# Optimization experiments

Hardware: AMD Instinct MI355X
Metric: run time of the kernel (lower is better)

## Reference

```python
import jax, jax.numpy as jnp
import numpy as np

B, S, D = 4, 2048, 1024
E, ES, K = 16, 256, 4  # n_experts, expert_size, top-k (= n_heads)
STD_GATE = 0.02


def setup_inputs() -> dict:
    key = jax.random.key(0)
    k1, k2, k3, k4 = jax.random.split(key, 4)
    x = jax.random.normal(k1, (B, S, D), dtype=jnp.float32)
    # init per module: gate ~ N(0, d^-0.5), keys ~ N(0, d^-0.5), values ~ N(0, size^-0.5)
    w_gate = jax.random.normal(k2, (E, D), dtype=jnp.float32) * (D ** -0.5)
    keys = jax.random.normal(k3, (E, D, ES), dtype=jnp.float32) * (D ** -0.5)
    values = jax.random.normal(k4, (E, ES, D), dtype=jnp.float32) * ((E * ES) ** -0.5)
    return {"x": x, "w_gate": w_gate, "keys": keys, "values": values}


def reference(x, w_gate, keys, values):
    # sigma-MoE forward (selection_mode='sigmoid', activation=relu,
    # num_selected = n_heads = K, no bias, no dropout, eval mode)
    xt = x.reshape(-1, D)                         # [T, D]
    T = xt.shape[0]
    logits = xt @ w_gate.T                        # [T, E]
    sel = jax.nn.sigmoid(logits)                  # sigmoid gating
    sel_val, sel_idx = jax.lax.top_k(sel, K)      # [T, K]
    # sparse gate weights as dense [T, E] mask (zeros for unselected experts)
    gate_w = jnp.zeros((T, E), dtype=x.dtype).at[
        jnp.arange(T)[:, None], sel_idx
    ].set(sel_val)
    # per-expert hidden: h[t,e,s] = relu(sum_d x[t,d] keys[e,d,s])
    h = jax.nn.relu(jnp.einsum('td,eds->tes', xt, keys))  # [T, E, ES]
    # weighted scatter back through values: out = sum_e gate * h_e @ values_e
    out = jnp.einsum('tes,te,esv->tv', h, gate_w, values)  # [T, D]
    return out.reshape(B, S, D)
```

## Files before the change

### kernel.cpp

```cpp
#include <hip/hip_runtime.h>
#include <hip/hip_bf16.h>
#include <stdint.h>

#define T_TOK 8192
#define DIM   1024
#define NEXP  16
#define ESZ   256
#define TOPK  4
#define BM    128
#define BK    64
#define NPAIR (T_TOK*TOPK)
#define NBLK  128
#define MAXROWS (T_TOK*TOPK + NEXP*BM)
#define MAXTILES (T_TOK*TOPK/BM + NEXP)

typedef __hip_bfloat16 bf16;
typedef short bf16x8 __attribute__((ext_vector_type(8)));
typedef float f32x4 __attribute__((ext_vector_type(4)));

__device__ __forceinline__ unsigned short f2bu(float f){
  __hip_bfloat16 b = __float2bfloat16(f);
  return *reinterpret_cast<unsigned short*>(&b);
}
__device__ __forceinline__ float bu2f(unsigned short u){
  __hip_bfloat16 b = *reinterpret_cast<__hip_bfloat16*>(&u);
  return __bfloat162float(b);
}

__device__ __forceinline__ void gload16(const void* g, void* l){
  __builtin_amdgcn_global_load_lds((const __attribute__((address_space(1))) void*)g,
                                   (__attribute__((address_space(3))) void*)l, 16, 0, 0);
}

__global__ __launch_bounds__(256) void k_gate(const float* __restrict__ x,
    const float* __restrict__ wg, bf16* __restrict__ xb,
    int* __restrict__ sel_idx, float* __restrict__ sel_gate)
{
  const int wave = threadIdx.x >> 6, lane = threadIdx.x & 63;
  const int t = blockIdx.x*4 + wave;
  const float* xr = x + (size_t)t*DIM;
  float4 xv[4];
#pragma unroll
  for (int c=0;c<4;c++) xv[c] = *(const float4*)(xr + c*256 + lane*4);
#pragma unroll
  for (int c=0;c<4;c++){
    ushort4 o; o.x=f2bu(xv[c].x); o.y=f2bu(xv[c].y); o.z=f2bu(xv[c].z); o.w=f2bu(xv[c].w);
    *(ushort4*)((unsigned short*)xb + (size_t)t*DIM + c*256 + lane*4) = o;
  }
  float sg[NEXP];
#pragma unroll
  for (int e=0;e<NEXP;e++){
    const float* wr = wg + e*DIM;
    float p = 0.f;
#pragma unroll
    for (int c=0;c<4;c++){
      float4 w = *(const float4*)(wr + c*256 + lane*4);
      p += xv[c].x*w.x + xv[c].y*w.y + xv[c].z*w.z + xv[c].w*w.w;
    }
#pragma unroll
    for (int s=1;s<64;s<<=1) p += __shfl_xor(p, s);
    sg[e] = 1.f/(1.f + expf(-p));
  }
  if (lane==0){
    unsigned chosen = 0;
#pragma unroll
    for (int k=0;k<TOPK;k++){
      float best=-1.f; int bi=0;
#pragma unroll
      for (int e=0;e<NEXP;e++){
        float v = ((chosen>>e)&1u) ? -2.f : sg[e];
        if (v>best){best=v;bi=e;}
      }
      chosen |= 1u<<bi;
      sel_idx[t*TOPK+k]=bi; sel_gate[t*TOPK+k]=best;
    }
  }
}

__global__ __launch_bounds__(256) void k_transpose2(const float* __restrict__ keys,
    const float* __restrict__ values, bf16* __restrict__ kT, bf16* __restrict__ vT)
{
  __shared__ float tile[32][33];
  const int which = blockIdx.y >> 4, e = blockIdx.y & 15;
  const int R = which ? ESZ : DIM, C = which ? DIM : ESZ;
  const float* src = (which ? values : keys) + (size_t)e*DIM*ESZ;
  bf16* dst = (which ? vT : kT) + (size_t)e*DIM*ESZ;
  const int ctiles = C/32;
  const int r0 = (blockIdx.x / ctiles)*32, c0 = (blockIdx.x % ctiles)*32;
  const int tx = threadIdx.x & 31, ty = threadIdx.x >> 5;
#pragma unroll
  for (int i=0;i<4;i++){ int r = ty + i*8; tile[r][tx] = src[(size_t)(r0+r)*C + c0 + tx]; }
  __syncthreads();
#pragma unroll
  for (int i=0;i<4;i++){ int r = ty + i*8; dst[(size_t)(c0+r)*R + r0 + tx] = __float2bfloat16(tile[tx][r]); }
}

__global__ __launch_bounds__(256) void k_hist(const int* __restrict__ sel_idx,
    int* __restrict__ block_hist)
{
  __shared__ int h[NEXP];
  if (threadIdx.x < NEXP) h[threadIdx.x]=0;
  __syncthreads();
  atomicAdd(&h[sel_idx[blockIdx.x*256 + threadIdx.x]], 1);
  __syncthreads();
  if (threadIdx.x < NEXP) block_hist[blockIdx.x*NEXP + threadIdx.x] = h[threadIdx.x];
}

__global__ void k_meta(const int* __restrict__ block_hist,
    int* __restrict__ tile_expert, int* __restrict__ tile_rowstart,
    int* __restrict__ tile_segend, int* __restrict__ block_base)
{
  __shared__ int cnt[NEXP], seg[NEXP];
  const int tid = threadIdx.x;
  if (tid < NEXP){
    int s=0;
    for (int b=0;b<NBLK;b++) s += block_hist[b*NEXP + tid];
    cnt[tid]=s;
  }
  __syncthreads();
  if (tid==0){
    int off=0, tc=0;
    for (int e=0;e<NEXP;e++){
      seg[e]=off;
      int c = cnt[e];
      int nt = (c + BM - 1)/BM;
      for (int i=0;i<nt;i++){
        tile_expert[tc]=e; tile_rowstart[tc]=off+i*BM; tile_segend[tc]=off+c; tc++;
      }
      off += nt*BM;
    }
    for (; tc<MAXTILES; tc++) tile_expert[tc]=-1;
  }
  __syncthreads();
  if (tid < NEXP){
    int s = seg[tid];
    for (int b=0;b<NBLK;b++){ block_base[b*NEXP + tid] = s; s += block_hist[b*NEXP + tid]; }
  }
}

__global__ __launch_bounds__(256) void k_scatter(const int* __restrict__ sel_idx,
    const float* __restrict__ sel_gate, const int* __restrict__ block_base,
    int* __restrict__ assign_token, float* __restrict__ assign_gate,
    int* __restrict__ inv_rows)
{
  __shared__ int wcnt[4][NEXP];
  const int p = blockIdx.x*256 + threadIdx.x;
  const int wave = threadIdx.x >> 6, lane = threadIdx.x & 63;
  const int e = sel_idx[p];
  const float g = sel_gate[p];
  int rank = 0;
#pragma unroll
  for (int ee=0; ee<NEXP; ee++){
    unsigned long long m = __ballot(e==ee);
    if (lane==0) wcnt[wave][ee] = (int)__popcll(m);
    if (e==ee) rank = (int)__popcll(m & ((1ull<<lane)-1ull));
  }
  __syncthreads();
  int pre = 0;
  for (int w=0; w<wave; w++) pre += wcnt[w][e];
  const int row = block_base[blockIdx.x*NEXP + e] + pre + rank;
  assign_token[row] = p >> 2;
  assign_gate[row]  = g;
  inv_rows[p] = row;
}

__global__ __launch_bounds__(256) void k_gemm1(
    const bf16* __restrict__ xb, const bf16* __restrict__ kT,
    const int* __restrict__ assign_token, const float* __restrict__ assign_gate,
    const int* __restrict__ tile_expert, const int* __restrict__ tile_rowstart,
    const int* __restrict__ tile_segend, bf16* __restrict__ h)
{
  __shared__ char smem[65536];
  __shared__ int   tokens_s[BM];
  __shared__ float gates_s[BM];

  const int nb = blockIdx.x, tile = blockIdx.y;
  const int e = tile_expert[tile];
  if (e < 0) return;
  const int row0 = tile_rowstart[tile];
  const int segend = tile_segend[tile];
  const int tid = threadIdx.x, wave = tid>>6, lane = tid&63;

  if (tid < BM){
    int rg = row0 + tid;
    bool vld = rg < segend;
    tokens_s[tid] = vld ? assign_token[rg] : 0;
    gates_s[tid]  = vld ? assign_gate[rg] : 0.f;
  }
  __syncthreads();

  char* As = smem;
  char* Bs = smem + 32768;
  const bf16* gA[4]; const bf16* gB[4]; int lo[4];
#pragma unroll
  for (int i=0;i<4;i++){
    int rl = (wave*4+i)*8 + (lane>>3);
    int c  = (lane&7) ^ (rl&7);
    gA[i] = xb + (size_t)tokens_s[rl]*DIM + c*8;
    gB[i] = kT + ((size_t)e*ESZ + nb*BM + rl)*DIM + c*8;
    lo[i] = (wave*4+i)*1024;
  }

  f32x4 acc[4][4];
#pragma unroll
  for (int m=0;m<4;m++)
#pragma unroll
    for (int n=0;n<4;n++) acc[m][n] = {0.f,0.f,0.f,0.f};

  const int wr0 = (wave>>1)*64, wc0 = (wave&1)*64;
  const int NT = DIM/BK;

#pragma unroll
  for (int i=0;i<4;i++){ gload16(gA[i], As + lo[i]); gload16(gB[i], Bs + lo[i]); }
  asm volatile("s_waitcnt vmcnt(0)" ::: "memory");
  __builtin_amdgcn_s_barrier();

  for (int kt=0; kt<NT; ++kt){
    const int cur = kt & 1;
    if (kt+1 < NT){
      const int nxt = cur^1;
#pragma unroll
      for (int i=0;i<4;i++){
        gload16(gA[i] + (kt+1)*BK, As + nxt*16384 + lo[i]);
        gload16(gB[i] + (kt+1)*BK, Bs + nxt*16384 + lo[i]);
      }
    }
    const char* Ab = As + cur*16384; const char* Bb = Bs + cur*16384;
#pragma unroll
    for (int kk=0;kk<2;kk++){
      bf16x8 af[4], bfr[4];
#pragma unroll
      for (int m=0;m<4;m++){
        int row = wr0 + m*16 + (lane&15);
        int kb  = kk*64 + (lane>>4)*16;
        af[m] = *(const bf16x8*)(Ab + row*128 + (kb ^ ((row&7)<<4)));
      }
#pragma unroll
      for (int n=0;n<4;n++){
        int col = wc0 + n*16 + (lane&15);
        int kb  = kk*64 + (lane>>4)*16;
        bfr[n] = *(const bf16x8*)(Bb + col*128 + (kb ^ ((col&7)<<4)));
      }
#pragma unroll
      for (int m=0;m<4;m++)
#pragma unroll
        for (int n=0;n<4;n++)
          acc[m][n] = __builtin_amdgcn_mfma_f32_16x16x32_bf16(af[m], bfr[n], acc[m][n], 0,0,0);
    }
    asm volatile("s_waitcnt vmcnt(0)" ::: "memory");
    __builtin_amdgcn_s_barrier();
  }

#pragma unroll
  for (int m=0;m<4;m++)
#pragma unroll
    for (int n=0;n<4;n++){
      int col = wc0 + n*16 + (lane&15);
#pragma unroll
      for (int j=0;j<4;j++){
        int rloc = wr0 + m*16 + ((lane>>4)<<2) + j;
        float v = fmaxf(acc[m][n][j], 0.f) * gates_s[rloc];
        h[(size_t)(row0 + rloc)*ESZ + nb*BM + col] = __float2bfloat16(v);
      }
    }
}

__global__ __launch_bounds__(256) void k_gemm2(
    const bf16* __restrict__ h, const bf16* __restrict__ vT,
    const int* __restrict__ tile_expert, const int* __restrict__ tile_rowstart,
    bf16* __restrict__ partial)
{
  __shared__ char smem[65536];

  const int nb = blockIdx.x, tile = blockIdx.y;
  const int e = tile_expert[tile];
  if (e < 0) return;
  const int row0 = tile_rowstart[tile];
  const int tid = threadIdx.x, wave = tid>>6, lane = tid&63;

  char* As = smem;
  char* Bs = smem + 32768;
  const bf16* gA[4]; const bf16* gB[4]; int lo[4];
#pragma unroll
  for (int i=0;i<4;i++){
    int rl = (wave*4+i)*8 + (lane>>3);
    int c  = (lane&7) ^ (rl&7);
    gA[i] = h + (size_t)(row0 + rl)*ESZ + c*8;
    gB[i] = vT + ((size_t)e*DIM + nb*BM + rl)*ESZ + c*8;
    lo[i] = (wave*4+i)*1024;
  }

  f32x4 acc[4][4];
#pragma unroll
  for (int m=0;m<4;m++)
#pragma unroll
    for (int n=0;n<4;n++) acc[m][n] = {0.f,0.f,0.f,0.f};

  const int wr0 = (wave>>1)*64, wc0 = (wave&1)*64;
  const int NT = ESZ/BK;

#pragma unroll
  for (int i=0;i<4;i++){ gload16(gA[i], As + lo[i]); gload16(gB[i], Bs + lo[i]); }
  asm volatile("s_waitcnt vmcnt(0)" ::: "memory");
  __builtin_amdgcn_s_barrier();

  for (int kt=0; kt<NT; ++kt){
    const int cur = kt & 1;
    if (kt+1 < NT){
      const int nxt = cur^1;
#pragma unroll
      for (int i=0;i<4;i++){
        gload16(gA[i] + (kt+1)*BK, As + nxt*16384 + lo[i]);
        gload16(gB[i] + (kt+1)*BK, Bs + nxt*16384 + lo[i]);
      }
    }
    const char* Ab = As + cur*16384; const char* Bb = Bs + cur*16384;
#pragma unroll
    for (int kk=0;kk<2;kk++){
      bf16x8 af[4], bfr[4];
#pragma unroll
      for (int m=0;m<4;m++){
        int row = wr0 + m*16 + (lane&15);
        int kb  = kk*64 + (lane>>4)*16;
        af[m] = *(const bf16x8*)(Ab + row*128 + (kb ^ ((row&7)<<4)));
      }
#pragma unroll
      for (int n=0;n<4;n++){
        int col = wc0 + n*16 + (lane&15);
        int kb  = kk*64 + (lane>>4)*16;
        bfr[n] = *(const bf16x8*)(Bb + col*128 + (kb ^ ((col&7)<<4)));
      }
#pragma unroll
      for (int m=0;m<4;m++)
#pragma unroll
        for (int n=0;n<4;n++)
          acc[m][n] = __builtin_amdgcn_mfma_f32_16x16x32_bf16(af[m], bfr[n], acc[m][n], 0,0,0);
    }
    asm volatile("s_waitcnt vmcnt(0)" ::: "memory");
    __builtin_amdgcn_s_barrier();
  }

#pragma unroll
  for (int m=0;m<4;m++)
#pragma unroll
    for (int n=0;n<4;n++){
      int col = wc0 + n*16 + (lane&15);
#pragma unroll
      for (int j=0;j<4;j++){
        int rloc = wr0 + m*16 + ((lane>>4)<<2) + j;
        partial[(size_t)(row0 + rloc)*DIM + nb*BM + col] = __float2bfloat16(acc[m][n][j]);
      }
    }
}

__global__ __launch_bounds__(256) void k_reduce(const bf16* __restrict__ partial,
    const int* __restrict__ inv_rows, float* __restrict__ out)
{
  const int t = blockIdx.x;
  const int c0 = threadIdx.x * 4;
  int rows[TOPK];
#pragma unroll
  for (int k=0;k<TOPK;k++) rows[k] = inv_rows[t*TOPK+k];
  float a0=0.f,a1=0.f,a2=0.f,a3=0.f;
#pragma unroll
  for (int k=0;k<TOPK;k++){
    ushort4 v = *(const ushort4*)((const unsigned short*)partial + (size_t)rows[k]*DIM + c0);
    a0 += bu2f(v.x); a1 += bu2f(v.y); a2 += bu2f(v.z); a3 += bu2f(v.w);
  }
  float4 o = {a0,a1,a2,a3};
  *(float4*)(out + (size_t)t*DIM + c0) = o;
}

extern "C" void kernel_launch(void* const* d_in, const int* in_sizes, int n_in,
                              void* d_out, int out_size, void* d_ws, size_t ws_size,
                              hipStream_t stream)
{
  const float* x      = (const float*)d_in[0];
  const float* wg     = (const float*)d_in[1];
  const float* keys   = (const float*)d_in[2];
  const float* values = (const float*)d_in[3];
  float* out = (float*)d_out;

  char* ws = (char*)d_ws;
  size_t off = 0;
  bf16* vT   = (bf16*)(ws+off); off += (size_t)NEXP*DIM*ESZ*2;
  bf16* hbuf = (bf16*)(ws+off); off += (size_t)MAXROWS*ESZ*2;
  int*   sel_idx      = (int*)  (ws+off); off += (size_t)NPAIR*4;
  float* sel_gate     = (float*)(ws+off); off += (size_t)NPAIR*4;
  int*   assign_token = (int*)  (ws+off); off += (size_t)MAXROWS*4;
  float* assign_gate  = (float*)(ws+off); off += (size_t)MAXROWS*4;
  int*   inv_rows     = (int*)  (ws+off); off += (size_t)NPAIR*4;
  int*   block_hist   = (int*)  (ws+off); off += (size_t)NBLK*NEXP*4;
  int*   block_base   = (int*)  (ws+off); off += (size_t)NBLK*NEXP*4;
  int*   tile_expert  = (int*)  (ws+off); off += 4096;
  int*   tile_rowstart= (int*)  (ws+off); off += 4096;
  int*   tile_segend  = (int*)  (ws+off); off += 4096;
  const size_t PARTIAL_BYTES = (size_t)MAXROWS*DIM*2;
  const size_t XB_BYTES = (size_t)T_TOK*DIM*2;
  const size_t KT_BYTES = (size_t)NEXP*ESZ*DIM*2;
  bf16* partial = (bf16*)(ws+off); off += PARTIAL_BYTES;
  bf16* xb = (bf16*)((char*)partial + PARTIAL_BYTES - XB_BYTES - KT_BYTES);
  bf16* kT = (bf16*)((char*)partial + PARTIAL_BYTES - KT_BYTES);

  k_gate<<<T_TOK/4, 256, 0, stream>>>(x, wg, xb, sel_idx, sel_gate);
  k_transpose2<<<dim3(256, NEXP*2), 256, 0, stream>>>(keys, values, kT, vT);
  k_hist<<<NBLK, 256, 0, stream>>>(sel_idx, block_hist);
  k_meta<<<1, 256, 0, stream>>>(block_hist, tile_expert, tile_rowstart, tile_segend, block_base);
  k_scatter<<<NBLK, 256, 0, stream>>>(sel_idx, sel_gate, block_base, assign_token,
      assign_gate, inv_rows);
  k_gemm1<<<dim3(ESZ/BM, MAXTILES), 256, 0, stream>>>(xb, kT, assign_token, assign_gate,
      tile_expert, tile_rowstart, tile_segend, hbuf);
  k_gemm2<<<dim3(DIM/BM, MAXTILES), 256, 0, stream>>>(hbuf, vT,
      tile_expert, tile_rowstart, partial);
  k_reduce<<<T_TOK, 256, 0, stream>>>(partial, inv_rows, out);
}
```

Before: 164.6 us.

## Fuse expert up and down GEMMs into one kernel keeping hidden tile in LDS

Merges the two grouped GEMM kernels into a single 512-thread kernel. Each block computes the full 128x256 hidden tile for its expert, applies relu and the gate, stores it swizzled in shared memory, then streams the value weights to produce all 1024 output columns. This removes the global round trip of the hidden buffer and the recomputation of token gathers across column blocks. In exchange each block needs 96KB of LDS, so fewer blocks fit per CU and there is less parallelism per tile. It also remaps tile indices for scheduling.

```diff
diff --git a/kernel.cpp b/kernel.cpp
--- a/kernel.cpp
+++ b/kernel.cpp
@@ -164,17 +164,19 @@
   inv_rows[p] = row;
 }
 
-__global__ __launch_bounds__(256) void k_gemm1(
+__global__ __launch_bounds__(512) void k_expert(
     const bf16* __restrict__ xb, const bf16* __restrict__ kT,
+    const bf16* __restrict__ vT,
     const int* __restrict__ assign_token, const float* __restrict__ assign_gate,
     const int* __restrict__ tile_expert, const int* __restrict__ tile_rowstart,
-    const int* __restrict__ tile_segend, bf16* __restrict__ h)
-{
-  __shared__ char smem[65536];
+    const int* __restrict__ tile_segend, bf16* __restrict__ partial)
+{
+  __shared__ char smem[98304];
   __shared__ int   tokens_s[BM];
   __shared__ float gates_s[BM];
 
-  const int nb = blockIdx.x, tile = blockIdx.y;
+  const int bid = blockIdx.x;
+  const int tile = (bid & 7)*34 + (bid >> 3);
   const int e = tile_expert[tile];
   if (e < 0) return;
   const int row0 = tile_rowstart[tile];
@@ -185,20 +187,28 @@
     int rg = row0 + tid;
     bool vld = rg < segend;
     tokens_s[tid] = vld ? assign_token[rg] : 0;
-    gates_s[tid]  = vld ? assign_gate[rg] : 0.f;
+    gates_s[tid]  = vld ? assign_gate[rg]  : 0.f;
   }
   __syncthreads();
 
   char* As = smem;
   char* Bs = smem + 32768;
-  const bf16* gA[4]; const bf16* gB[4]; int lo[4];
+
+  const bf16* gA[2]; int loA[2];
+#pragma unroll
+  for (int i=0;i<2;i++){
+    int r = wave*16 + i*8 + (lane>>3);
+    int c = (lane&7) ^ (r&7);
+    gA[i] = xb + (size_t)tokens_s[r]*DIM + c*8;
+    loA[i] = (wave*2+i)*1024;
+  }
+  const bf16* gB[4]; int loB[4];
 #pragma unroll
   for (int i=0;i<4;i++){
-    int rl = (wave*4+i)*8 + (lane>>3);
-    int c  = (lane&7) ^ (rl&7);
-    gA[i] = xb + (size_t)tokens_s[rl]*DIM + c*8;
-    gB[i] = kT + ((size_t)e*ESZ + nb*BM + rl)*DIM + c*8;
-    lo[i] = (wave*4+i)*1024;
+    int col = wave*32 + i*8 + (lane>>3);
+    int c = (lane&7) ^ (col&7);
+    gB[i] = kT + ((size_t)e*ESZ + col)*DIM + c*8;
+    loB[i] = (wave*4+i)*1024;
   }
 
   f32x4 acc[4][4];
@@ -207,25 +217,26 @@
 #pragma unroll
     for (int n=0;n<4;n++) acc[m][n] = {0.f,0.f,0.f,0.f};
 
-  const int wr0 = (wave>>1)*64, wc0 = (wave&1)*64;
-  const int NT = DIM/BK;
-
-#pragma unroll
-  for (int i=0;i<4;i++){ gload16(gA[i], As + lo[i]); gload16(gB[i], Bs + lo[i]); }
+  const int wr0 = (wave>>2)*64, wc0 = (wave&3)*64;
+
+#pragma unroll
+  for (int i=0;i<2;i++) gload16(gA[i], As + loA[i]);
+#pragma unroll
+  for (int i=0;i<4;i++) gload16(gB[i], Bs + loB[i]);
   asm volatile("s_waitcnt vmcnt(0)" ::: "memory");
   __builtin_amdgcn_s_barrier();
 
-  for (int kt=0; kt<NT; ++kt){
+  for (int kt=0; kt<16; ++kt){
     const int cur = kt & 1;
-    if (kt+1 < NT){
+    if (kt < 15){
       const int nxt = cur^1;
 #pragma unroll
-      for (int i=0;i<4;i++){
-        gload16(gA[i] + (kt+1)*BK, As + nxt*16384 + lo[i]);
-        gload16(gB[i] + (kt+1)*BK, Bs + nxt*16384 + lo[i]);
-      }
-    }
-    const char* Ab = As + cur*16384; const char* Bb = Bs + cur*16384;
+      for (int i=0;i<2;i++) gload16(gA[i] + (kt+1)*BK, As + nxt*16384 + loA[i]);
+#pragma unroll
+      for (int i=0;i<4;i++) gload16(gB[i] + (kt+1)*BK, Bs + nxt*32768 + loB[i]);
+    }
+    const char* Ab = As + cur*16384;
+    const char* Bb = Bs + cur*32768;
 #pragma unroll
     for (int kk=0;kk<2;kk++){
       bf16x8 af[4], bfr[4];
@@ -251,6 +262,19 @@
     __builtin_amdgcn_s_barrier();
   }
 
+  char* h_s = smem;
+  char* Vs  = smem + 65536;
+  const bf16* gV[2]; int loV[2];
+#pragma unroll
+  for (int i=0;i<2;i++){
+    int vr = wave*16 + i*8 + (lane>>3);
+    int c  = (lane&7) ^ (vr&7);
+    gV[i] = vT + ((size_t)e*DIM + vr)*ESZ + c*8;
+    loV[i] = (wave*2+i)*1024;
+  }
+#pragma unroll
+  for (int i=0;i<2;i++) gload16(gV[i], Vs + loV[i]);
+
 #pragma unroll
   for (int m=0;m<4;m++)
 #pragma unroll
@@ -258,99 +282,71 @@
       int col = wc0 + n*16 + (lane&15);
 #pragma unroll
       for (int j=0;j<4;j++){
-        int rloc = wr0 + m*16 + ((lane>>4)<<2) + j;
-        float v = fmaxf(acc[m][n][j], 0.f) * gates_s[rloc];
-        h[(size_t)(row0 + rloc)*ESZ + nb*BM + col] = __float2bfloat16(v);
-      }
-    }
-}
-
-__global__ __launch_bounds__(256) void k_gemm2(
-    const bf16* __restrict__ h, const bf16* __restrict__ vT,
-    const int* __restrict__ tile_expert, const int* __restrict__ tile_rowstart,
-    bf16* __restrict__ partial)
-{
-  __shared__ char smem[65536];
-
-  const int nb = blockIdx.x, tile = blockIdx.y;
-  const int e = tile_expert[tile];
-  if (e < 0) return;
-  const int row0 = tile_rowstart[tile];
-  const int tid = threadIdx.x, wave = tid>>6, lane = tid&63;
-
-  char* As = smem;
-  char* Bs = smem + 32768;
-  const bf16* gA[4]; const bf16* gB[4]; int lo[4];
-#pragma unroll
-  for (int i=0;i<4;i++){
-    int rl = (wave*4+i)*8 + (lane>>3);
-    int c  = (lane&7) ^ (rl&7);
-    gA[i] = h + (size_t)(row0 + rl)*ESZ + c*8;
-    gB[i] = vT + ((size_t)e*DIM + nb*BM + rl)*ESZ + c*8;
-    lo[i] = (wave*4+i)*1024;
-  }
-
-  f32x4 acc[4][4];
+        int row = wr0 + m*16 + ((lane>>4)<<2) + j;
+        float v = fmaxf(acc[m][n][j], 0.f) * gates_s[row];
+        *(unsigned short*)(h_s + row*512 + ((col*2) ^ ((row&7)<<4))) = f2bu(v);
+      }
+    }
+  asm volatile("s_waitcnt vmcnt(0) lgkmcnt(0)" ::: "memory");
+  __builtin_amdgcn_s_barrier();
+
+  f32x4 acc2[4][2];
 #pragma unroll
   for (int m=0;m<4;m++)
 #pragma unroll
-    for (int n=0;n<4;n++) acc[m][n] = {0.f,0.f,0.f,0.f};
-
-  const int wr0 = (wave>>1)*64, wc0 = (wave&1)*64;
-  const int NT = ESZ/BK;
-
-#pragma unroll
-  for (int i=0;i<4;i++){ gload16(gA[i], As + lo[i]); gload16(gB[i], Bs + lo[i]); }
-  asm volatile("s_waitcnt vmcnt(0)" ::: "memory");
-  __builtin_amdgcn_s_barrier();
-
-  for (int kt=0; kt<NT; ++kt){
-    const int cur = kt & 1;
-    if (kt+1 < NT){
+    for (int n=0;n<2;n++) acc2[m][n] = {0.f,0.f,0.f,0.f};
+  const int qr0 = (wave>>2)*64;
+  const int qc0 = (wave&3)*32;
+
+  for (int s=0; s<32; ++s){
+    const int cur = s & 1;
+    if (s+1 < 32){
       const int nxt = cur^1;
-#pragma unroll
-      for (int i=0;i<4;i++){
-        gload16(gA[i] + (kt+1)*BK, As + nxt*16384 + lo[i]);
-        gload16(gB[i] + (kt+1)*BK, Bs + nxt*16384 + lo[i]);
-      }
-    }
-    const char* Ab = As + cur*16384; const char* Bb = Bs + cur*16384;
+      const int off = ((s+1)>>2)*32768 + ((s+1)&3)*64;
+#pragma unroll
+      for (int i=0;i<2;i++) gload16(gV[i] + off, Vs + nxt*16384 + loV[i]);
+    }
+    const char* Vb = Vs + cur*16384;
+    const int kt = s & 3;
 #pragma unroll
     for (int kk=0;kk<2;kk++){
-      bf16x8 af[4], bfr[4];
+      bf16x8 af[4], bfr[2];
 #pragma unroll
       for (int m=0;m<4;m++){
-        int row = wr0 + m*16 + (lane&15);
-        int kb  = kk*64 + (lane>>4)*16;
-        af[m] = *(const bf16x8*)(Ab + row*128 + (kb ^ ((row&7)<<4)));
-      }
-#pragma unroll
-      for (int n=0;n<4;n++){
-        int col = wc0 + n*16 + (lane&15);
-        int kb  = kk*64 + (lane>>4)*16;
-        bfr[n] = *(const bf16x8*)(Bb + col*128 + (kb ^ ((col&7)<<4)));
+        int vr = qr0 + m*16 + (lane&15);
+        int kb = kk*64 + (lane>>4)*16;
+        af[m] = *(const bf16x8*)(Vb + vr*128 + (kb ^ ((vr&7)<<4)));
+      }
+#pragma unroll
+      for (int n=0;n<2;n++){
+        int tok = qc0 + n*16 + (lane&15);
+        int hb  = kt*128 + kk*64 + (lane>>4)*16;
+        bfr[n] = *(const bf16x8*)(h_s + tok*512 + (hb ^ ((tok&7)<<4)));
       }
 #pragma unroll
       for (int m=0;m<4;m++)
 #pragma unroll
-        for (int n=0;n<4;n++)
-          acc[m][n] = __builtin_amdgcn_mfma_f32_16x16x32_bf16(af[m], bfr[n], acc[m][n], 0,0,0);
+        for (int n=0;n<2;n++)
+          acc2[m][n] = __builtin_amdgcn_mfma_f32_16x16x32_bf16(af[m], bfr[n], acc2[m][n], 0,0,0);
+    }
+    if (kt == 3){
+      const int chunk = s >> 2;
+#pragma unroll
+      for (int m=0;m<4;m++)
+#pragma unroll
+        for (int n=0;n<2;n++){
+          int tok = qc0 + n*16 + (lane&15);
+          int od  = chunk*128 + qr0 + m*16 + ((lane>>4)<<2);
+          ushort4 o;
+          o.x = f2bu(acc2[m][n][0]); o.y = f2bu(acc2[m][n][1]);
+          o.z = f2bu(acc2[m][n][2]); o.w = f2bu(acc2[m][n][3]);
+          *(ushort4*)((unsigned short*)partial + (size_t)(row0+tok)*DIM + od) = o;
+          acc2[m][n] = {0.f,0.f,0.f,0.f};
+        }
     }
     asm volatile("s_waitcnt vmcnt(0)" ::: "memory");
     __builtin_amdgcn_s_barrier();
   }
-
-#pragma unroll
-  for (int m=0;m<4;m++)
-#pragma unroll
-    for (int n=0;n<4;n++){
-      int col = wc0 + n*16 + (lane&15);
-#pragma unroll
-      for (int j=0;j<4;j++){
-        int rloc = wr0 + m*16 + ((lane>>4)<<2) + j;
-        partial[(size_t)(row0 + rloc)*DIM + nb*BM + col] = __float2bfloat16(acc[m][n][j]);
-      }
-    }
 }
 
 __global__ __launch_bounds__(256) void k_reduce(const bf16* __restrict__ partial,
@@ -384,7 +380,8 @@
   char* ws = (char*)d_ws;
   size_t off = 0;
   bf16* vT   = (bf16*)(ws+off); off += (size_t)NEXP*DIM*ESZ*2;
-  bf16* hbuf = (bf16*)(ws+off); off += (size_t)MAXROWS*ESZ*2;
+  bf16* kT   = (bf16*)(ws+off); off += (size_t)NEXP*ESZ*DIM*2;
+  bf16* xb   = (bf16*)(ws+off); off += (size_t)T_TOK*DIM*2;
   int*   sel_idx      = (int*)  (ws+off); off += (size_t)NPAIR*4;
   float* sel_gate     = (float*)(ws+off); off += (size_t)NPAIR*4;
   int*   assign_token = (int*)  (ws+off); off += (size_t)MAXROWS*4;
@@ -395,12 +392,7 @@
   int*   tile_expert  = (int*)  (ws+off); off += 4096;
   int*   tile_rowstart= (int*)  (ws+off); off += 4096;
   int*   tile_segend  = (int*)  (ws+off); off += 4096;
-  const size_t PARTIAL_BYTES = (size_t)MAXROWS*DIM*2;
-  const size_t XB_BYTES = (size_t)T_TOK*DIM*2;
-  const size_t KT_BYTES = (size_t)NEXP*ESZ*DIM*2;
-  bf16* partial = (bf16*)(ws+off); off += PARTIAL_BYTES;
-  bf16* xb = (bf16*)((char*)partial + PARTIAL_BYTES - XB_BYTES - KT_BYTES);
-  bf16* kT = (bf16*)((char*)partial + PARTIAL_BYTES - KT_BYTES);
+  bf16* partial = (bf16*)(ws+off); off += (size_t)MAXROWS*DIM*2;
 
   k_gate<<<T_TOK/4, 256, 0, stream>>>(x, wg, xb, sel_idx, sel_gate);
   k_transpose2<<<dim3(256, NEXP*2), 256, 0, stream>>>(keys, values, kT, vT);
@@ -408,9 +400,7 @@
   k_meta<<<1, 256, 0, stream>>>(block_hist, tile_expert, tile_rowstart, tile_segend, block_base);
   k_scatter<<<NBLK, 256, 0, stream>>>(sel_idx, sel_gate, block_base, assign_token,
       assign_gate, inv_rows);
-  k_gemm1<<<dim3(ESZ/BM, MAXTILES), 256, 0, stream>>>(xb, kT, assign_token, assign_gate,
-      tile_expert, tile_rowstart, tile_segend, hbuf);
-  k_gemm2<<<dim3(DIM/BM, MAXTILES), 256, 0, stream>>>(hbuf, vT,
-      tile_expert, tile_rowstart, partial);
+  k_expert<<<MAXTILES, 512, 0, stream>>>(xb, kT, vT, assign_token, assign_gate,
+      tile_expert, tile_rowstart, tile_segend, partial);
   k_reduce<<<T_TOK, 256, 0, stream>>>(partial, inv_rows, out);
 }
```

Measured after the change: 202.3 us. 1.23x slower.

## Fuse expert histogram into gate kernel and restructure GEMM double-buffer loops

Applied to the files above, without the earlier changes.

The per-block expert histogram now comes from the gating kernel through shared-memory atomics, so the separate histogram launch is removed. The meta kernel folds groups of 16 gate-block histograms back into the 128 scatter-block bases. Both grouped GEMMs get a manually unrolled ping-pong loop with fixed LDS buffer addresses, precomputed swizzled LDS offsets, and incremented global pointers, which cuts per-iteration address arithmetic. In exchange, the meta kernel reads a larger histogram array, and the gate kernel adds a barrier and atomics.

```diff
diff --git a/kernel.cpp b/kernel.cpp
--- a/kernel.cpp
+++ b/kernel.cpp
@@ -10,6 +10,7 @@
 #define BM    128
 #define BK    64
 #define NPAIR (T_TOK*TOPK)
+#define NGB   (T_TOK/4)
 #define NBLK  128
 #define MAXROWS (T_TOK*TOPK + NEXP*BM)
 #define MAXTILES (T_TOK*TOPK/BM + NEXP)
@@ -34,8 +35,13 @@
 
 __global__ __launch_bounds__(256) void k_gate(const float* __restrict__ x,
     const float* __restrict__ wg, bf16* __restrict__ xb,
-    int* __restrict__ sel_idx, float* __restrict__ sel_gate)
-{
+    int* __restrict__ sel_idx, float* __restrict__ sel_gate,
+    int* __restrict__ block_hist)
+{
+  __shared__ int h[NEXP];
+  if (threadIdx.x < NEXP) h[threadIdx.x] = 0;
+  __syncthreads();
+
   const int wave = threadIdx.x >> 6, lane = threadIdx.x & 63;
   const int t = blockIdx.x*4 + wave;
   const float* xr = x + (size_t)t*DIM;
@@ -73,8 +79,11 @@
       }
       chosen |= 1u<<bi;
       sel_idx[t*TOPK+k]=bi; sel_gate[t*TOPK+k]=best;
-    }
-  }
+      atomicAdd(&h[bi], 1);
+    }
+  }
+  __syncthreads();
+  if (threadIdx.x < NEXP) block_hist[blockIdx.x*NEXP + threadIdx.x] = h[threadIdx.x];
 }
 
 __global__ __launch_bounds__(256) void k_transpose2(const float* __restrict__ keys,
@@ -95,26 +104,24 @@
   for (int i=0;i<4;i++){ int r = ty + i*8; dst[(size_t)(c0+r)*R + r0 + tx] = __float2bfloat16(tile[tx][r]); }
 }
 
-__global__ __launch_bounds__(256) void k_hist(const int* __restrict__ sel_idx,
-    int* __restrict__ block_hist)
-{
-  __shared__ int h[NEXP];
-  if (threadIdx.x < NEXP) h[threadIdx.x]=0;
-  __syncthreads();
-  atomicAdd(&h[sel_idx[blockIdx.x*256 + threadIdx.x]], 1);
-  __syncthreads();
-  if (threadIdx.x < NEXP) block_hist[blockIdx.x*NEXP + threadIdx.x] = h[threadIdx.x];
-}
-
-__global__ void k_meta(const int* __restrict__ block_hist,
+__global__ void k_meta(const int* __restrict__ gh,
     int* __restrict__ tile_expert, int* __restrict__ tile_rowstart,
     int* __restrict__ tile_segend, int* __restrict__ block_base)
 {
+  __shared__ int sbc[NBLK][NEXP];
   __shared__ int cnt[NEXP], seg[NEXP];
   const int tid = threadIdx.x;
+  for (int cell = tid; cell < NBLK*NEXP; cell += 256){
+    int sb = cell >> 4, e = cell & 15;
+    int s = 0;
+#pragma unroll
+    for (int g=0; g<16; ++g) s += gh[(sb*16+g)*NEXP + e];
+    sbc[sb][e] = s;
+  }
+  __syncthreads();
   if (tid < NEXP){
     int s=0;
-    for (int b=0;b<NBLK;b++) s += block_hist[b*NEXP + tid];
+    for (int sb=0; sb<NBLK; sb++) s += sbc[sb][tid];
     cnt[tid]=s;
   }
   __syncthreads();
@@ -134,7 +141,7 @@
   __syncthreads();
   if (tid < NEXP){
     int s = seg[tid];
-    for (int b=0;b<NBLK;b++){ block_base[b*NEXP + tid] = s; s += block_hist[b*NEXP + tid]; }
+    for (int sb=0; sb<NBLK; sb++){ block_base[sb*NEXP + tid] = s; s += sbc[sb][tid]; }
   }
 }
 
@@ -189,64 +196,65 @@
   }
   __syncthreads();
 
-  char* As = smem;
-  char* Bs = smem + 32768;
-  const bf16* gA[4]; const bf16* gB[4]; int lo[4];
+  const bf16* qA[4]; const bf16* qB[4]; int lo[4];
 #pragma unroll
   for (int i=0;i<4;i++){
     int rl = (wave*4+i)*8 + (lane>>3);
     int c  = (lane&7) ^ (rl&7);
-    gA[i] = xb + (size_t)tokens_s[rl]*DIM + c*8;
-    gB[i] = kT + ((size_t)e*ESZ + nb*BM + rl)*DIM + c*8;
+    qA[i] = xb + (size_t)tokens_s[rl]*DIM + c*8;
+    qB[i] = kT + ((size_t)e*ESZ + nb*BM + rl)*DIM + c*8;
     lo[i] = (wave*4+i)*1024;
   }
 
+  const int wr0 = (wave>>1)*64, wc0 = (wave&1)*64;
+  int offA[2][4], offB[2][4];
+#pragma unroll
+  for (int kk=0;kk<2;kk++){
+    int kb = kk*64 + (lane>>4)*16;
+#pragma unroll
+    for (int m=0;m<4;m++){ int row = wr0 + m*16 + (lane&15); offA[kk][m] = row*128 + (kb ^ ((row&7)<<4)); }
+#pragma unroll
+    for (int n=0;n<4;n++){ int col = wc0 + n*16 + (lane&15); offB[kk][n] = col*128 + (kb ^ ((col&7)<<4)); }
+  }
+
   f32x4 acc[4][4];
 #pragma unroll
   for (int m=0;m<4;m++)
 #pragma unroll
     for (int n=0;n<4;n++) acc[m][n] = {0.f,0.f,0.f,0.f};
 
-  const int wr0 = (wave>>1)*64, wc0 = (wave&1)*64;
-  const int NT = DIM/BK;
-
-#pragma unroll
-  for (int i=0;i<4;i++){ gload16(gA[i], As + lo[i]); gload16(gB[i], Bs + lo[i]); }
+  auto compute = [&](const char* Ab, const char* Bb){
+#pragma unroll
+    for (int kk=0;kk<2;kk++){
+      bf16x8 af[4], bfr[4];
+#pragma unroll
+      for (int m=0;m<4;m++) af[m]  = *(const bf16x8*)(Ab + offA[kk][m]);
+#pragma unroll
+      for (int n=0;n<4;n++) bfr[n] = *(const bf16x8*)(Bb + offB[kk][n]);
+#pragma unroll
+      for (int m=0;m<4;m++)
+#pragma unroll
+        for (int n=0;n<4;n++)
+          acc[m][n] = __builtin_amdgcn_mfma_f32_16x16x32_bf16(af[m], bfr[n], acc[m][n], 0,0,0);
+    }
+  };
+
+#pragma unroll
+  for (int i=0;i<4;i++){ gload16(qA[i], smem+lo[i]); gload16(qB[i], smem+32768+lo[i]); qA[i]+=BK; qB[i]+=BK; }
   asm volatile("s_waitcnt vmcnt(0)" ::: "memory");
   __builtin_amdgcn_s_barrier();
 
-  for (int kt=0; kt<NT; ++kt){
-    const int cur = kt & 1;
-    if (kt+1 < NT){
-      const int nxt = cur^1;
-#pragma unroll
-      for (int i=0;i<4;i++){
-        gload16(gA[i] + (kt+1)*BK, As + nxt*16384 + lo[i]);
-        gload16(gB[i] + (kt+1)*BK, Bs + nxt*16384 + lo[i]);
-      }
-    }
-    const char* Ab = As + cur*16384; const char* Bb = Bs + cur*16384;
-#pragma unroll
-    for (int kk=0;kk<2;kk++){
-      bf16x8 af[4], bfr[4];
-#pragma unroll
-      for (int m=0;m<4;m++){
-        int row = wr0 + m*16 + (lane&15);
-        int kb  = kk*64 + (lane>>4)*16;
-        af[m] = *(const bf16x8*)(Ab + row*128 + (kb ^ ((row&7)<<4)));
-      }
-#pragma unroll
-      for (int n=0;n<4;n++){
-        int col = wc0 + n*16 + (lane&15);
-        int kb  = kk*64 + (lane>>4)*16;
-        bfr[n] = *(const bf16x8*)(Bb + col*128 + (kb ^ ((col&7)<<4)));
-      }
-#pragma unroll
-      for (int m=0;m<4;m++)
-#pragma unroll
-        for (int n=0;n<4;n++)
-          acc[m][n] = __builtin_amdgcn_mfma_f32_16x16x32_bf16(af[m], bfr[n], acc[m][n], 0,0,0);
-    }
+  for (int kt=0; kt<16; kt+=2){
+#pragma unroll
+    for (int i=0;i<4;i++){ gload16(qA[i], smem+16384+lo[i]); gload16(qB[i], smem+49152+lo[i]); qA[i]+=BK; qB[i]+=BK; }
+    compute(smem, smem+32768);
+    asm volatile("s_waitcnt vmcnt(0)" ::: "memory");
+    __builtin_amdgcn_s_barrier();
+    if (kt+2 < 16){
+#pragma unroll
+      for (int i=0;i<4;i++){ gload16(qA[i], smem+lo[i]); gload16(qB[i], smem+32768+lo[i]); qA[i]+=BK; qB[i]+=BK; }
+    }
+    compute(smem+16384, smem+49152);
     asm volatile("s_waitcnt vmcnt(0)" ::: "memory");
     __builtin_amdgcn_s_barrier();
   }
@@ -278,64 +286,65 @@
   const int row0 = tile_rowstart[tile];
   const int tid = threadIdx.x, wave = tid>>6, lane = tid&63;
 
-  char* As = smem;
-  char* Bs = smem + 32768;
-  const bf16* gA[4]; const bf16* gB[4]; int lo[4];
+  const bf16* qA[4]; const bf16* qB[4]; int lo[4];
 #pragma unroll
   for (int i=0;i<4;i++){
     int rl = (wave*4+i)*8 + (lane>>3);
     int c  = (lane&7) ^ (rl&7);
-    gA[i] = h + (size_t)(row0 + rl)*ESZ + c*8;
-    gB[i] = vT + ((size_t)e*DIM + nb*BM + rl)*ESZ + c*8;
+    qA[i] = h + (size_t)(row0 + rl)*ESZ + c*8;
+    qB[i] = vT + ((size_t)e*DIM + nb*BM + rl)*ESZ + c*8;
     lo[i] = (wave*4+i)*1024;
   }
 
+  const int wr0 = (wave>>1)*64, wc0 = (wave&1)*64;
+  int offA[2][4], offB[2][4];
+#pragma unroll
+  for (int kk=0;kk<2;kk++){
+    int kb = kk*64 + (lane>>4)*16;
+#pragma unroll
+    for (int m=0;m<4;m++){ int row = wr0 + m*16 + (lane&15); offA[kk][m] = row*128 + (kb ^ ((row&7)<<4)); }
+#pragma unroll
+    for (int n=0;n<4;n++){ int col = wc0 + n*16 + (lane&15); offB[kk][n] = col*128 + (kb ^ ((col&7)<<4)); }
+  }
+
   f32x4 acc[4][4];
 #pragma unroll
   for (int m=0;m<4;m++)
 #pragma unroll
     for (int n=0;n<4;n++) acc[m][n] = {0.f,0.f,0.f,0.f};
 
-  const int wr0 = (wave>>1)*64, wc0 = (wave&1)*64;
-  const int NT = ESZ/BK;
-
-#pragma unroll
-  for (int i=0;i<4;i++){ gload16(gA[i], As + lo[i]); gload16(gB[i], Bs + lo[i]); }
+  auto compute = [&](const char* Ab, const char* Bb){
+#pragma unroll
+    for (int kk=0;kk<2;kk++){
+      bf16x8 af[4], bfr[4];
+#pragma unroll
+      for (int m=0;m<4;m++) af[m]  = *(const bf16x8*)(Ab + offA[kk][m]);
+#pragma unroll
+      for (int n=0;n<4;n++) bfr[n] = *(const bf16x8*)(Bb + offB[kk][n]);
+#pragma unroll
+      for (int m=0;m<4;m++)
+#pragma unroll
+        for (int n=0;n<4;n++)
+          acc[m][n] = __builtin_amdgcn_mfma_f32_16x16x32_bf16(af[m], bfr[n], acc[m][n], 0,0,0);
+    }
+  };
+
+#pragma unroll
+  for (int i=0;i<4;i++){ gload16(qA[i], smem+lo[i]); gload16(qB[i], smem+32768+lo[i]); qA[i]+=BK; qB[i]+=BK; }
   asm volatile("s_waitcnt vmcnt(0)" ::: "memory");
   __builtin_amdgcn_s_barrier();
 
-  for (int kt=0; kt<NT; ++kt){
-    const int cur = kt & 1;
-    if (kt+1 < NT){
-      const int nxt = cur^1;
-#pragma unroll
-      for (int i=0;i<4;i++){
-        gload16(gA[i] + (kt+1)*BK, As + nxt*16384 + lo[i]);
-        gload16(gB[i] + (kt+1)*BK, Bs + nxt*16384 + lo[i]);
-      }
-    }
-    const char* Ab = As + cur*16384; const char* Bb = Bs + cur*16384;
-#pragma unroll
-    for (int kk=0;kk<2;kk++){
-      bf16x8 af[4], bfr[4];
-#pragma unroll
-      for (int m=0;m<4;m++){
-        int row = wr0 + m*16 + (lane&15);
-        int kb  = kk*64 + (lane>>4)*16;
-        af[m] = *(const bf16x8*)(Ab + row*128 + (kb ^ ((row&7)<<4)));
-      }
-#pragma unroll
-      for (int n=0;n<4;n++){
-        int col = wc0 + n*16 + (lane&15);
-        int kb  = kk*64 + (lane>>4)*16;
-        bfr[n] = *(const bf16x8*)(Bb + col*128 + (kb ^ ((col&7)<<4)));
-      }
-#pragma unroll
-      for (int m=0;m<4;m++)
-#pragma unroll
-        for (int n=0;n<4;n++)
-          acc[m][n] = __builtin_amdgcn_mfma_f32_16x16x32_bf16(af[m], bfr[n], acc[m][n], 0,0,0);
-    }
+  for (int kt=0; kt<4; kt+=2){
+#pragma unroll
+    for (int i=0;i<4;i++){ gload16(qA[i], smem+16384+lo[i]); gload16(qB[i], smem+49152+lo[i]); qA[i]+=BK; qB[i]+=BK; }
+    compute(smem, smem+32768);
+    asm volatile("s_waitcnt vmcnt(0)" ::: "memory");
+    __builtin_amdgcn_s_barrier();
+    if (kt+2 < 4){
+#pragma unroll
+      for (int i=0;i<4;i++){ gload16(qA[i], smem+lo[i]); gload16(qB[i], smem+32768+lo[i]); qA[i]+=BK; qB[i]+=BK; }
+    }
+    compute(smem+16384, smem+49152);
     asm volatile("s_waitcnt vmcnt(0)" ::: "memory");
     __builtin_amdgcn_s_barrier();
   }
@@ -390,7 +399,7 @@
   int*   assign_token = (int*)  (ws+off); off += (size_t)MAXROWS*4;
   float* assign_gate  = (float*)(ws+off); off += (size_t)MAXROWS*4;
   int*   inv_rows     = (int*)  (ws+off); off += (size_t)NPAIR*4;
-  int*   block_hist   = (int*)  (ws+off); off += (size_t)NBLK*NEXP*4;
+  int*   block_hist   = (int*)  (ws+off); off += (size_t)NGB*NEXP*4;
   int*   block_base   = (int*)  (ws+off); off += (size_t)NBLK*NEXP*4;
   int*   tile_expert  = (int*)  (ws+off); off += 4096;
   int*   tile_rowstart= (int*)  (ws+off); off += 4096;
@@ -402,9 +411,8 @@
   bf16* xb = (bf16*)((char*)partial + PARTIAL_BYTES - XB_BYTES - KT_BYTES);
   bf16* kT = (bf16*)((char*)partial + PARTIAL_BYTES - KT_BYTES);
 
-  k_gate<<<T_TOK/4, 256, 0, stream>>>(x, wg, xb, sel_idx, sel_gate);
+  k_gate<<<NGB, 256, 0, stream>>>(x, wg, xb, sel_idx, sel_gate, block_hist);
   k_transpose2<<<dim3(256, NEXP*2), 256, 0, stream>>>(keys, values, kT, vT);
-  k_hist<<<NBLK, 256, 0, stream>>>(sel_idx, block_hist);
   k_meta<<<1, 256, 0, stream>>>(block_hist, tile_expert, tile_rowstart, tile_segend, block_base);
   k_scatter<<<NBLK, 256, 0, stream>>>(sel_idx, sel_gate, block_base, assign_token,
       assign_gate, inv_rows);
```

New measurement: 168.7 us. +2.5%, slower.
